# Kernel tuning notes

Measured on AMD Instinct MI355X. Metric: run time of the kernel, lower is better.

## Reference

```python
import jax, jax.numpy as jnp
import numpy as np

A_BITS = 7   # activation - 1, per T_quantize(norm(x), activation-1)
W_BITS = 7   # weight quantization levels bits (IRlinear, bit=weight)
HEADS = 16
DIM_HEAD = 64
LN_EPS = 1e-5


def qfn(x, bit):
    """Symmetric per-tensor uniform quantization with straight-through estimator.
    bit >= 31 means bypass (fp path, matching weight/activation == 32 defaults)."""
    if bit >= 31:
        return x
    n = jnp.asarray(2.0 ** bit - 1.0, x.dtype)
    s = jnp.max(jnp.abs(x))
    s = jnp.where(s == 0, jnp.asarray(1.0, x.dtype), s)
    y = jnp.round(x / s * n) / n * s
    # STE: forward uses quantized value, gradient passes through unchanged
    return x + jax.lax.stop_gradient(y - x)


def setup_inputs() -> dict:
    key = jax.random.key(0)
    kx, kq, ko = jax.random.split(key, 3)
    B, N, C = 8, 1024, 1024
    inner = HEADS * DIM_HEAD  # 1024
    x = jax.random.normal(kx, (B, N, C), dtype=jnp.float32)
    gamma = jnp.ones((C,), dtype=jnp.float32)
    beta = jnp.zeros((C,), dtype=jnp.float32)
    W_qkv = jax.random.normal(kq, (3 * inner, C), dtype=jnp.float32) * 0.02
    W_out = jax.random.normal(ko, (C, inner), dtype=jnp.float32) * 0.02
    b_out = jnp.zeros((C,), dtype=jnp.float32)
    return {"x": x, "gamma": gamma, "beta": beta,
            "W_qkv": W_qkv, "W_out": W_out, "b_out": b_out}


def reference(x, gamma, beta, W_qkv, W_out, b_out):
    B, N, C = x.shape
    H, Dh = HEADS, DIM_HEAD
    # LayerNorm
    mu = jnp.mean(x, axis=-1, keepdims=True)
    var = jnp.mean(jnp.square(x - mu), axis=-1, keepdims=True)
    xn = (x - mu) * jax.lax.rsqrt(var + LN_EPS) * gamma + beta
    # activation quantization (T_quantize with activation-1 bits)
    xq = qfn(xn, A_BITS)
    # quantized QKV projection (IRlinear, no bias)
    qkv = jnp.einsum('bnc,oc->bno', xq, qfn(W_qkv, W_BITS))
    qkv = qkv.reshape(B, N, 3, H, Dh).transpose(2, 0, 3, 1, 4)  # [3,B,H,N,Dh]
    q, k, v = qkv[0], qkv[1], qkv[2]
    # scaled dot-product attention (dropout_p = 0)
    scale = Dh ** -0.5
    scores = jnp.einsum('bhqd,bhkd->bhqk', q, k) * scale
    attn = jax.nn.softmax(scores, axis=-1)
    o = jnp.einsum('bhqk,bhkd->bhqd', attn, v)  # [B,H,N,Dh]
    o = o.transpose(0, 2, 1, 3).reshape(B, N, H * Dh)
    # quantized output projection (IRlinear, with bias)
    out = jnp.einsum('bni,ci->bnc', o, qfn(W_out, W_BITS)) + b_out
    return out
```

## Files before the change

kernel.cpp:

```cpp
#include <hip/hip_runtime.h>
#include <hip/hip_bf16.h>
#include <math.h>

typedef unsigned int u32;
typedef unsigned short u16;
using f32x4  = __attribute__((ext_vector_type(4))) float;
using f32x16 = __attribute__((ext_vector_type(16))) float;
using bfrag  = __attribute__((ext_vector_type(8))) short;
using i32x4  = __attribute__((ext_vector_type(4))) int;
union FragU { uint4 u; bfrag f; };
union FragI { uint4 u; i32x4 f; };

#define HEADS 16
#define DH    64
#define NB    8
#define NN    1024
#define NC    1024
#define M_TOT 8192
#define O_QKV 3072
#define KDIM  1024
#define LOG2E 1.44269504088896340736f

static __device__ __forceinline__ u16 f2bf(float f) {
  u32 u = __float_as_uint(f);
  return (u16)((u + 0x7fffu + ((u >> 16) & 1u)) >> 16);
}
static __device__ __forceinline__ u32 pk_bf16(float a, float b) {
  __hip_bfloat162 h = __float22bfloat162_rn(make_float2(a, b));
  u32 r; __builtin_memcpy(&r, &h, 4); return r;
}

static __device__ __forceinline__ float wave_sum(float v) {
#pragma unroll
  for (int off = 32; off > 0; off >>= 1) v += __shfl_xor(v, off, 64);
  return v;
}
static __device__ __forceinline__ float wave_max(float v) {
#pragma unroll
  for (int off = 32; off > 0; off >>= 1) v = fmaxf(v, __shfl_xor(v, off, 64));
  return v;
}

static __device__ __forceinline__ f32x4 mfma16(FragU a, FragU b, f32x4 c) {
  return __builtin_amdgcn_mfma_f32_16x16x32_bf16(a.f, b.f, c, 0, 0, 0);
}
static __device__ __forceinline__ f32x16 mfma32(FragU a, FragU b, f32x16 c) {
  return __builtin_amdgcn_mfma_f32_32x32x16_bf16(a.f, b.f, c, 0, 0, 0);
}
static __device__ __forceinline__ i32x4 mfma16i(FragI a, FragI b, i32x4 c) {
  return __builtin_amdgcn_mfma_i32_16x16x64_i8(a.f, b.f, c, 0, 0, 0);
}

static __device__ __forceinline__ void pl32swap(u32& a, u32& b) {
#if __has_builtin(__builtin_amdgcn_permlane32_swap)
  using u32x2 = __attribute__((ext_vector_type(2))) unsigned int;
  u32x2 r = __builtin_amdgcn_permlane32_swap(a, b, false, false);
  a = r[0]; b = r[1];
#else
  asm volatile("v_permlane32_swap_b32 %0, %1" : "+v"(a), "+v"(b));
#endif
}

template<int P, int BLK>
static __device__ __forceinline__ void stage_rows(const char* g, int row_stride,
                                                  char* ldsb, int t) {
#pragma unroll
  for (int p = 0; p < P; ++p) {
    const int c = p * BLK + t;
    const int row = c >> 3, kc = c & 7;
    const char* gp = g + (size_t)row * row_stride + ((kc ^ (row & 7)) << 4);
    char* lp = ldsb + ((p * BLK + (t & ~63)) << 4);
    __builtin_amdgcn_global_load_lds((const __attribute__((address_space(1))) void*)gp,
                                     (__attribute__((address_space(3))) void*)lp, 16, 0, 0);
  }
}
static __device__ __forceinline__ uint4 ld_chunk(const char* base, int row, int chunk) {
  return *(const uint4*)(base + (((row << 3) + (chunk ^ (row & 7))) << 4));
}

__global__ __launch_bounds__(256) void prep_kernel(const float* __restrict__ x,
    const float* __restrict__ g, const float* __restrict__ b,
    const float4* __restrict__ wq, const float4* __restrict__ wo,
    float2* __restrict__ mrs, float* __restrict__ actp,
    float* __restrict__ wqp, float* __restrict__ wop)
{
  __shared__ float red[4];
  const int bid = blockIdx.x, t = threadIdx.x;
  if (bid < 2048) {
    const int w = t >> 6, l = t & 63;
    const int row = (bid << 2) + w;
    const float4* xr = (const float4*)(x + (size_t)row * NC);
    float4 v[4];
#pragma unroll
    for (int j = 0; j < 4; ++j) v[j] = xr[l + (j << 6)];
    float s = 0.f;
#pragma unroll
    for (int j = 0; j < 4; ++j) s += (v[j].x + v[j].y) + (v[j].z + v[j].w);
    s = wave_sum(s);
    const float mu = s * (1.0f / NC);
    float ss = 0.f;
#pragma unroll
    for (int j = 0; j < 4; ++j) {
      const float dx = v[j].x - mu, dy = v[j].y - mu, dz = v[j].z - mu, dw = v[j].w - mu;
      ss += (dx * dx + dy * dy) + (dz * dz + dw * dw);
    }
    ss = wave_sum(ss);
    const float rstd = 1.0f / sqrtf(ss * (1.0f / NC) + 1e-5f);
    if (l == 0) mrs[row] = make_float2(mu, rstd);
    float am = 0.f;
#pragma unroll
    for (int j = 0; j < 4; ++j) {
      const float4 gv = ((const float4*)g)[l + (j << 6)];
      const float4 bv = ((const float4*)b)[l + (j << 6)];
      const float yx = (v[j].x - mu) * rstd * gv.x + bv.x;
      const float yy = (v[j].y - mu) * rstd * gv.y + bv.y;
      const float yz = (v[j].z - mu) * rstd * gv.z + bv.z;
      const float yw = (v[j].w - mu) * rstd * gv.w + bv.w;
      am = fmaxf(am, fmaxf(fmaxf(fabsf(yx), fabsf(yy)), fmaxf(fabsf(yz), fabsf(yw))));
    }
    am = wave_max(am);
    if (l == 0) red[w] = am;
    __syncthreads();
    if (t == 0) actp[bid] = fmaxf(fmaxf(red[0], red[1]), fmaxf(red[2], red[3]));
  } else {
    const float4* p; int n4, lb, nb; float* o;
    if (bid < 2560) { p = wq; n4 = O_QKV * KDIM / 4; lb = bid - 2048; nb = 512; o = wqp + lb; }
    else            { p = wo; n4 = NC * KDIM / 4;    lb = bid - 2560; nb = 256; o = wop + lb; }
    float m = 0.f;
    for (int i = lb * 256 + t; i < n4; i += nb * 256) {
      float4 v = p[i];
      m = fmaxf(m, fmaxf(fmaxf(fabsf(v.x), fabsf(v.y)), fmaxf(fabsf(v.z), fabsf(v.w))));
    }
    m = wave_max(m);
    if ((t & 63) == 0) red[t >> 6] = m;
    __syncthreads();
    if (t == 0) *o = fmaxf(fmaxf(red[0], red[1]), fmaxf(red[2], red[3]));
  }
}

__global__ __launch_bounds__(256) void reduce3(const float* __restrict__ actp,
    const float* __restrict__ wqp, const float* __restrict__ wop,
    unsigned* __restrict__ scal)
{
  const int t = threadIdx.x;
  float a = 0.f, q = 0.f, o = 0.f;
#pragma unroll
  for (int k = 0; k < 8; ++k) a = fmaxf(a, actp[t + (k << 8)]);
  q = fmaxf(wqp[t], wqp[t + 256]);
  o = wop[t];
  a = wave_max(a); q = wave_max(q); o = wave_max(o);
  __shared__ float ra[4], rq[4], ro[4];
  if ((t & 63) == 0) { ra[t >> 6] = a; rq[t >> 6] = q; ro[t >> 6] = o; }
  __syncthreads();
  if (t == 0) {
    a = fmaxf(fmaxf(ra[0], ra[1]), fmaxf(ra[2], ra[3]));
    q = fmaxf(fmaxf(rq[0], rq[1]), fmaxf(rq[2], rq[3]));
    o = fmaxf(fmaxf(ro[0], ro[1]), fmaxf(ro[2], ro[3]));
    scal[0] = __float_as_uint(a == 0.f ? 1.f : a);
    scal[1] = __float_as_uint(q == 0.f ? 1.f : q);
    scal[2] = __float_as_uint(o == 0.f ? 1.f : o);
  }
}

__global__ __launch_bounds__(256) void quant_all(const float* __restrict__ x,
    const float* __restrict__ g, const float* __restrict__ b,
    const float2* __restrict__ mrs, const unsigned* __restrict__ scal,
    u32* __restrict__ xq, const float4* __restrict__ wq, u32* __restrict__ oq,
    const float4* __restrict__ wo, uint2* __restrict__ oo)
{
  const int bid = blockIdx.x, t = threadIdx.x;
  if (bid < 8192) {
    const long long row = bid;
    const float2 ms = mrs[row];
    const float s = __uint_as_float(scal[0]);
    const float4 v = ((const float4*)(x + row * NC))[t];
    const float4 gv = ((const float4*)g)[t];
    const float4 bv = ((const float4*)b)[t];
    float4 y;
    y.x = (v.x - ms.x) * ms.y * gv.x + bv.x;
    y.y = (v.y - ms.x) * ms.y * gv.y + bv.y;
    y.z = (v.z - ms.x) * ms.y * gv.z + bv.z;
    y.w = (v.w - ms.x) * ms.y * gv.w + bv.w;
    const int ia = (int)rintf(y.x / s * 127.0f);
    const int ib = (int)rintf(y.y / s * 127.0f);
    const int ic = (int)rintf(y.z / s * 127.0f);
    const int id = (int)rintf(y.w / s * 127.0f);
    xq[row * 256 + t] = (u32)(ia & 255) | ((u32)(ib & 255) << 8)
                      | ((u32)(ic & 255) << 16) | ((u32)(id & 255) << 24);
  } else if (bid < 8960) {
    const float s = __uint_as_float(scal[1]);
    const int base = (bid - 8192) << 10;
#pragma unroll
    for (int k = 0; k < 4; ++k) {
      const int i = base + (k << 8) + t;
      float4 v = wq[i];
      const int ia = (int)rintf(v.x / s * 127.0f);
      const int ib = (int)rintf(v.y / s * 127.0f);
      const int ic = (int)rintf(v.z / s * 127.0f);
      const int id = (int)rintf(v.w / s * 127.0f);
      oq[i] = (u32)(ia & 255) | ((u32)(ib & 255) << 8)
            | ((u32)(ic & 255) << 16) | ((u32)(id & 255) << 24);
    }
  } else {
    const float s = __uint_as_float(scal[2]);
    const int base = (bid - 8960) << 10;
#pragma unroll
    for (int k = 0; k < 4; ++k) {
      const int i = base + (k << 8) + t;
      float4 v = wo[i];
      uint2 o;
      o.x = pk_bf16(rintf(v.x / s * 127.0f), rintf(v.y / s * 127.0f));
      o.y = pk_bf16(rintf(v.z / s * 127.0f), rintf(v.w / s * 127.0f));
      oo[i] = o;
    }
  }
}

__global__ __launch_bounds__(256) void gemm_qkv_mfma(const char* __restrict__ A,
    const char* __restrict__ B, const unsigned* __restrict__ scal,
    u16* __restrict__ qp, u16* __restrict__ kp, u16* __restrict__ vtp)
{
  __shared__ __align__(16) char lds[32768];
  char* As = lds;
  char* Bs = lds + 16384;
  const int t = threadIdx.x, w = t >> 6, l = t & 63;
  const int lg = l >> 4, lc = l & 15;
  const int wm = (w >> 1) << 6, wn = (w & 1) << 6;
  i32x4 acc[4][4];
#pragma unroll
  for (int i = 0; i < 4; ++i)
#pragma unroll
    for (int j = 0; j < 4; ++j) acc[i][j] = 0;

  const char* gA = A + ((size_t)blockIdx.y << 7) * KDIM;
  const char* gB = B + ((size_t)blockIdx.x << 7) * KDIM;

  for (int k0 = 0; k0 < KDIM; k0 += 128) {
    stage_rows<4, 256>(gA + k0, KDIM, As, t);
    stage_rows<4, 256>(gB + k0, KDIM, Bs, t);
    __syncthreads();
#pragma unroll
    for (int ks = 0; ks < 2; ++ks) {
      FragI a[4], b[4];
#pragma unroll
      for (int mf = 0; mf < 4; ++mf) a[mf].u = ld_chunk(As, wm + (mf << 4) + lc, (ks << 2) + lg);
#pragma unroll
      for (int nf = 0; nf < 4; ++nf) b[nf].u = ld_chunk(Bs, wn + (nf << 4) + lc, (ks << 2) + lg);
      __builtin_amdgcn_s_setprio(1);
#pragma unroll
      for (int mf = 0; mf < 4; ++mf)
#pragma unroll
        for (int nf = 0; nf < 4; ++nf) acc[mf][nf] = mfma16i(a[mf], b[nf], acc[mf][nf]);
      __builtin_amdgcn_s_setprio(0);
    }
    __syncthreads();
  }

  const float sa = __uint_as_float(scal[0]), sw = __uint_as_float(scal[1]);
  const int which = blockIdx.x >> 3;
  float sc = sa * sw / 16129.0f;
  if (which == 0) sc *= 0.125f * LOG2E;
  const int obase = ((blockIdx.x & 7) << 7) + wn;
  const int mbase = ((int)blockIdx.y << 7) + wm;

  if (which < 2) {
    u16* d_ = which ? kp : qp;
#pragma unroll
    for (int nf = 0; nf < 4; ++nf) {
      const int od = obase + (nf << 4) + lc;
      const int hh = od >> 6, dd = od & 63;
#pragma unroll
      for (int mf = 0; mf < 4; ++mf)
#pragma unroll
        for (int r = 0; r < 4; ++r) {
          const int tok = mbase + (mf << 4) + (lg << 2) + r;
          const size_t addr = ((size_t)((tok >> 10) * HEADS + hh) << 16)
                            + ((size_t)(tok & 1023) << 6) + dd;
          d_[addr] = f2bf((float)acc[mf][nf][r] * sc);
        }
    }
  } else {
#pragma unroll
    for (int nf = 0; nf < 4; ++nf) {
      const int od = obase + (nf << 4) + lc;
      const int hh = od >> 6, dd = od & 63;
#pragma unroll
      for (int mf = 0; mf < 4; ++mf) {
        const int tok0 = mbase + (mf << 4) + (lg << 2);
        uint2 hv;
        hv.x = pk_bf16((float)acc[mf][nf][0] * sc, (float)acc[mf][nf][1] * sc);
        hv.y = pk_bf16((float)acc[mf][nf][2] * sc, (float)acc[mf][nf][3] * sc);
        const size_t base = ((size_t)((tok0 >> 10) * HEADS + hh) << 16)
                          + ((size_t)dd << 10) + (tok0 & 1023);
        *(uint2*)(vtp + base) = hv;
      }
    }
  }
}

__global__ __launch_bounds__(512) void attn_mfma(
    const u16* __restrict__ qp, const u16* __restrict__ kp, const u16* __restrict__ vtp,
    u16* __restrict__ ohp)
{
  __shared__ __align__(16) char lds[65536];
  const int t = threadIdx.x, w = t >> 6, l = t & 63;
  const int l31 = l & 31, h = l >> 5;
  const int id = blockIdx.x;
  const int bh = ((id & 7) << 4) + ((id >> 3) & 15);
  const int qbase = ((id >> 7) << 8) + (w << 5);
  const size_t bhoff = (size_t)bh << 16;

  FragU qf[4];
#pragma unroll
  for (int ks = 0; ks < 4; ++ks)
    qf[ks].u = *(const uint4*)(qp + bhoff + ((size_t)(qbase + l31) << 6) + (ks << 4) + (h << 3));

  f32x16 oacc[2];
  oacc[0] = 0.f; oacc[1] = 0.f;
  float lpart = 0.f;

  stage_rows<2, 512>((const char*)(kp + bhoff), 128, lds, t);
  stage_rows<1, 512>((const char*)(vtp + bhoff), 2048, lds + 16384, t);
  stage_rows<1, 512>((const char*)(vtp + bhoff + 64), 2048, lds + 24576, t);
  __syncthreads();

  for (int kb = 0; kb < 8; ++kb) {
    char* cur = lds + ((kb & 1) << 15);
    if (kb < 7) {
      char* nxt = lds + (((kb + 1) & 1) << 15);
      const size_t kn = kb + 1;
      stage_rows<2, 512>((const char*)(kp + bhoff + (kn << 13)), 128, nxt, t);
      stage_rows<1, 512>((const char*)(vtp + bhoff + (kn << 7)), 2048, nxt + 16384, t);
      stage_rows<1, 512>((const char*)(vtp + bhoff + (kn << 7) + 64), 2048, nxt + 24576, t);
    }

#pragma unroll
    for (int sub = 0; sub < 4; ++sub) {
      f32x16 s = 0.f;
#pragma unroll
      for (int ks = 0; ks < 4; ++ks) {
        FragU kf;
        kf.u = ld_chunk(cur, (sub << 5) + l31, (ks << 1) + h);
        __builtin_amdgcn_s_setprio(1);
        s = mfma32(kf, qf[ks], s);
        __builtin_amdgcn_s_setprio(0);
      }

      u32 W[8];
      float lsum = 0.f;
#pragma unroll
      for (int j = 0; j < 8; ++j) {
        const float a = __builtin_amdgcn_exp2f(s[2 * j]);
        const float b = __builtin_amdgcn_exp2f(s[2 * j + 1]);
        lsum += a + b;
        W[j] = pk_bf16(a, b);
      }
      lpart += lsum;

      FragU pf[2];
#pragma unroll
      for (int kk = 0; kk < 2; ++kk) {
        u32 a0 = W[4 * kk + 0], b0 = W[4 * kk + 2];
        u32 a1 = W[4 * kk + 1], b1 = W[4 * kk + 3];
        pl32swap(a0, b0); pl32swap(a1, b1);
        pf[kk].u = make_uint4(a0, a1, b0, b1);
      }

      char* Vh = cur + 16384 + ((sub >> 1) << 13);
#pragma unroll
      for (int ks = 0; ks < 2; ++ks)
#pragma unroll
        for (int dt = 0; dt < 2; ++dt) {
          FragU vf;
          vf.u = ld_chunk(Vh, (dt << 5) + l31, ((sub & 1) << 2) + (ks << 1) + h);
          __builtin_amdgcn_s_setprio(1);
          oacc[dt] = mfma32(vf, pf[ks], oacc[dt]);
          __builtin_amdgcn_s_setprio(0);
        }
    }
    __syncthreads();
  }

  lpart += __shfl_xor(lpart, 32, 64);
  const float invl = 1.0f / lpart;

  const int b = bh >> 4, hd_ = bh & 15;
  const size_t orow = (size_t)b * NN + qbase + l31;
  u16* ohb = ohp + (orow << 10) + (hd_ << 6);
#pragma unroll
  for (int dt = 0; dt < 2; ++dt)
#pragma unroll
    for (int rg = 0; rg < 4; ++rg) {
      const int d0 = (dt << 5) + (rg << 3) + (h << 2);
      const float v0 = oacc[dt][4 * rg + 0] * invl, v1 = oacc[dt][4 * rg + 1] * invl;
      const float v2 = oacc[dt][4 * rg + 2] * invl, v3 = oacc[dt][4 * rg + 3] * invl;
      uint2 hv;
      hv.x = (u32)f2bf(v0) | ((u32)f2bf(v1) << 16);
      hv.y = (u32)f2bf(v2) | ((u32)f2bf(v3) << 16);
      *(uint2*)(ohb + d0) = hv;
    }
}

__global__ __launch_bounds__(256) void gemm_out_mfma(const u16* __restrict__ Ah,
    const u16* __restrict__ B, const unsigned* __restrict__ scal,
    const float* __restrict__ bias, float* __restrict__ out)
{
  __shared__ __align__(16) char lds[32768];
  char* Ahs = lds;
  char* Bs  = lds + 16384;
  const int t = threadIdx.x, w = t >> 6, l = t & 63;
  const int lg = l >> 4, lc = l & 15;
  const int wm = (w >> 1) << 6, wn = (w & 1) << 6;
  f32x4 acc[4][4];
#pragma unroll
  for (int i = 0; i < 4; ++i)
#pragma unroll
    for (int j = 0; j < 4; ++j) acc[i][j] = 0.f;

  const char* gAh = (const char*)Ah + ((size_t)blockIdx.y << 7) * 2048;
  const char* gB  = (const char*)B  + ((size_t)blockIdx.x << 7) * 2048;

  for (int k0 = 0; k0 < KDIM; k0 += 64) {
    stage_rows<4, 256>(gAh + k0 * 2, 2048, Ahs, t);
    stage_rows<4, 256>(gB  + k0 * 2, 2048, Bs,  t);
    __syncthreads();
#pragma unroll
    for (int ks = 0; ks < 2; ++ks) {
      FragU a[4], b[4];
#pragma unroll
      for (int mf = 0; mf < 4; ++mf) a[mf].u = ld_chunk(Ahs, wm + (mf << 4) + lc, (ks << 2) + lg);
#pragma unroll
      for (int nf = 0; nf < 4; ++nf) b[nf].u = ld_chunk(Bs, wn + (nf << 4) + lc, (ks << 2) + lg);
      __builtin_amdgcn_s_setprio(1);
#pragma unroll
      for (int mf = 0; mf < 4; ++mf)
#pragma unroll
        for (int nf = 0; nf < 4; ++nf) acc[mf][nf] = mfma16(a[mf], b[nf], acc[mf][nf]);
      __builtin_amdgcn_s_setprio(0);
    }
    __syncthreads();
  }

  const float sc = __uint_as_float(scal[2]) / 127.0f;
  const int cb = ((int)blockIdx.x << 7) + wn;
  const int mb = ((int)blockIdx.y << 7) + wm;
#pragma unroll
  for (int nf = 0; nf < 4; ++nf) {
    const int col = cb + (nf << 4) + lc;
    const float bv = bias[col];
#pragma unroll
    for (int mf = 0; mf < 4; ++mf)
#pragma unroll
      for (int r = 0; r < 4; ++r) {
        const int row = mb + (mf << 4) + (lg << 2) + r;
        out[(size_t)row * NC + col] = acc[mf][nf][r] * sc + bv;
      }
  }
}

__global__ void ws_fail_kernel(float* out) { out[0] = 1.0e6f; }

extern "C" void kernel_launch(void* const* d_in, const int* in_sizes, int n_in,
                              void* d_out, int out_size, void* d_ws, size_t ws_size,
                              hipStream_t stream) {
  const float* x     = (const float*)d_in[0];
  const float* gamma = (const float*)d_in[1];
  const float* beta  = (const float*)d_in[2];
  const float* Wqkv  = (const float*)d_in[3];
  const float* Wout  = (const float*)d_in[4];
  const float* bout  = (const float*)d_in[5];
  float* out = (float*)d_out;

  char* ws = (char*)d_ws;
  unsigned* scal = (unsigned*)ws;
  size_t off = 256;
  float* actp = (float*)(ws + off); off += 2048 * 4;
  float* wqp  = (float*)(ws + off); off += 512 * 4;
  float* wop  = (float*)(ws + off); off += 256 * 4;
  off = (off + 255) & ~(size_t)255;
  float2* mrs = (float2*)(ws + off); off += (size_t)M_TOT * 8;
  char* xq  = ws + off; off += (size_t)M_TOT * KDIM;
  char* wqi = ws + off; off += (size_t)O_QKV * KDIM;
  u16* woi = (u16*)(ws + off); off += (size_t)NC * KDIM * 2;
  u16* qb  = (u16*)(ws + off); off += 16777216;
  u16* kb  = (u16*)(ws + off); off += 16777216;
  u16* vtb = (u16*)(ws + off); off += 16777216;
  u16* oh  = (u16*)(ws + off); off += 16777216;
  if (ws_size < off) { ws_fail_kernel<<<1, 1, 0, stream>>>(out); return; }

  prep_kernel<<<2816, 256, 0, stream>>>(x, gamma, beta, (const float4*)Wqkv,
                                        (const float4*)Wout, mrs, actp, wqp, wop);
  reduce3<<<1, 256, 0, stream>>>(actp, wqp, wop, scal);
  quant_all<<<9216, 256, 0, stream>>>(x, gamma, beta, mrs, scal, (u32*)xq,
                                      (const float4*)Wqkv, (u32*)wqi,
                                      (const float4*)Wout, (uint2*)woi);

  dim3 g1(O_QKV / 128, M_TOT / 128);
  gemm_qkv_mfma<<<g1, 256, 0, stream>>>(xq, wqi, scal, qb, kb, vtb);

  attn_mfma<<<512, 512, 0, stream>>>(qb, kb, vtb, oh);

  dim3 g3(NC / 128, M_TOT / 128);
  gemm_out_mfma<<<g3, 256, 0, stream>>>(oh, woi, scal, bout, out);
}
```

Baseline: 139.2 us.

## Fold scale reduction into quant kernel, transpose Q/K MFMA for packed stores, stagger attention subtiles

Removes the separate single-block reduce3 launch: each quant_all block now redundantly reduces the partial maxima itself, and block 0 writes the scalars for the later GEMMs. The QKV GEMM swaps MFMA operand order for the Q/K outputs so each lane holds four consecutive head-dim values and can write packed 8-byte stores instead of scalar 2-byte stores. The attention kernel rotates the sub-tile order per wave, likely to spread LDS bank accesses. Each quant block now does extra redundant reduction reads, and a duplicated GEMM loop adds code size.

```diff
diff --git a/kernel.cpp b/kernel.cpp
--- a/kernel.cpp
+++ b/kernel.cpp
@@ -76,6 +76,19 @@
 }
 static __device__ __forceinline__ uint4 ld_chunk(const char* base, int row, int chunk) {
   return *(const uint4*)(base + (((row << 3) + (chunk ^ (row & 7))) << 4));
+}
+
+static __device__ __forceinline__ float blk_max4(const float4* p, int n4, int t, float* red) {
+  float m = 0.f;
+  for (int i = t; i < n4; i += 256) {
+    float4 v = p[i];
+    m = fmaxf(m, fmaxf(fmaxf(v.x, v.y), fmaxf(v.z, v.w)));
+  }
+  m = wave_max(m);
+  __syncthreads();
+  if ((t & 63) == 0) red[t >> 6] = m;
+  __syncthreads();
+  return fmaxf(fmaxf(red[0], red[1]), fmaxf(red[2], red[3]));
 }
 
 __global__ __launch_bounds__(256) void prep_kernel(const float* __restrict__ x,
@@ -138,41 +151,30 @@
   }
 }
 
-__global__ __launch_bounds__(256) void reduce3(const float* __restrict__ actp,
-    const float* __restrict__ wqp, const float* __restrict__ wop,
-    unsigned* __restrict__ scal)
-{
-  const int t = threadIdx.x;
-  float a = 0.f, q = 0.f, o = 0.f;
-#pragma unroll
-  for (int k = 0; k < 8; ++k) a = fmaxf(a, actp[t + (k << 8)]);
-  q = fmaxf(wqp[t], wqp[t + 256]);
-  o = wop[t];
-  a = wave_max(a); q = wave_max(q); o = wave_max(o);
-  __shared__ float ra[4], rq[4], ro[4];
-  if ((t & 63) == 0) { ra[t >> 6] = a; rq[t >> 6] = q; ro[t >> 6] = o; }
-  __syncthreads();
-  if (t == 0) {
-    a = fmaxf(fmaxf(ra[0], ra[1]), fmaxf(ra[2], ra[3]));
-    q = fmaxf(fmaxf(rq[0], rq[1]), fmaxf(rq[2], rq[3]));
-    o = fmaxf(fmaxf(ro[0], ro[1]), fmaxf(ro[2], ro[3]));
-    scal[0] = __float_as_uint(a == 0.f ? 1.f : a);
-    scal[1] = __float_as_uint(q == 0.f ? 1.f : q);
-    scal[2] = __float_as_uint(o == 0.f ? 1.f : o);
-  }
-}
-
 __global__ __launch_bounds__(256) void quant_all(const float* __restrict__ x,
     const float* __restrict__ g, const float* __restrict__ b,
-    const float2* __restrict__ mrs, const unsigned* __restrict__ scal,
+    const float2* __restrict__ mrs,
+    const float* __restrict__ actp, const float* __restrict__ wqp,
+    const float* __restrict__ wop, unsigned* __restrict__ scal,
     u32* __restrict__ xq, const float4* __restrict__ wq, u32* __restrict__ oq,
     const float4* __restrict__ wo, uint2* __restrict__ oo)
 {
+  __shared__ float red[4];
   const int bid = blockIdx.x, t = threadIdx.x;
   if (bid < 8192) {
+    float s = blk_max4((const float4*)actp, 512, t, red);
+    if (s == 0.f) s = 1.f;
+    if (bid == 0) {
+      float qm = blk_max4((const float4*)wqp, 128, t, red);
+      float om = blk_max4((const float4*)wop, 64, t, red);
+      if (t == 0) {
+        scal[0] = __float_as_uint(s);
+        scal[1] = __float_as_uint(qm == 0.f ? 1.f : qm);
+        scal[2] = __float_as_uint(om == 0.f ? 1.f : om);
+      }
+    }
     const long long row = bid;
     const float2 ms = mrs[row];
-    const float s = __uint_as_float(scal[0]);
     const float4 v = ((const float4*)(x + row * NC))[t];
     const float4 gv = ((const float4*)g)[t];
     const float4 bv = ((const float4*)b)[t];
@@ -188,7 +190,8 @@
     xq[row * 256 + t] = (u32)(ia & 255) | ((u32)(ib & 255) << 8)
                       | ((u32)(ic & 255) << 16) | ((u32)(id & 255) << 24);
   } else if (bid < 8960) {
-    const float s = __uint_as_float(scal[1]);
+    float s = blk_max4((const float4*)wqp, 128, t, red);
+    if (s == 0.f) s = 1.f;
     const int base = (bid - 8192) << 10;
 #pragma unroll
     for (int k = 0; k < 4; ++k) {
@@ -202,7 +205,8 @@
             | ((u32)(ic & 255) << 16) | ((u32)(id & 255) << 24);
     }
   } else {
-    const float s = __uint_as_float(scal[2]);
+    float s = blk_max4((const float4*)wop, 64, t, red);
+    if (s == 0.f) s = 1.f;
     const int base = (bid - 8960) << 10;
 #pragma unroll
     for (int k = 0; k < 4; ++k) {
@@ -226,6 +230,7 @@
   const int t = threadIdx.x, w = t >> 6, l = t & 63;
   const int lg = l >> 4, lc = l & 15;
   const int wm = (w >> 1) << 6, wn = (w & 1) << 6;
+  const int which = blockIdx.x >> 3;
   i32x4 acc[4][4];
 #pragma unroll
   for (int i = 0; i < 4; ++i)
@@ -235,29 +240,51 @@
   const char* gA = A + ((size_t)blockIdx.y << 7) * KDIM;
   const char* gB = B + ((size_t)blockIdx.x << 7) * KDIM;
 
-  for (int k0 = 0; k0 < KDIM; k0 += 128) {
-    stage_rows<4, 256>(gA + k0, KDIM, As, t);
-    stage_rows<4, 256>(gB + k0, KDIM, Bs, t);
-    __syncthreads();
-#pragma unroll
-    for (int ks = 0; ks < 2; ++ks) {
-      FragI a[4], b[4];
-#pragma unroll
-      for (int mf = 0; mf < 4; ++mf) a[mf].u = ld_chunk(As, wm + (mf << 4) + lc, (ks << 2) + lg);
-#pragma unroll
-      for (int nf = 0; nf < 4; ++nf) b[nf].u = ld_chunk(Bs, wn + (nf << 4) + lc, (ks << 2) + lg);
-      __builtin_amdgcn_s_setprio(1);
-#pragma unroll
-      for (int mf = 0; mf < 4; ++mf)
-#pragma unroll
-        for (int nf = 0; nf < 4; ++nf) acc[mf][nf] = mfma16i(a[mf], b[nf], acc[mf][nf]);
-      __builtin_amdgcn_s_setprio(0);
-    }
-    __syncthreads();
+  if (which < 2) {
+    for (int k0 = 0; k0 < KDIM; k0 += 128) {
+      stage_rows<4, 256>(gA + k0, KDIM, As, t);
+      stage_rows<4, 256>(gB + k0, KDIM, Bs, t);
+      __syncthreads();
+#pragma unroll
+      for (int ks = 0; ks < 2; ++ks) {
+        FragI a[4], b[4];
+#pragma unroll
+        for (int mf = 0; mf < 4; ++mf) a[mf].u = ld_chunk(As, wm + (mf << 4) + lc, (ks << 2) + lg);
+#pragma unroll
+        for (int nf = 0; nf < 4; ++nf) b[nf].u = ld_chunk(Bs, wn + (nf << 4) + lc, (ks << 2) + lg);
+        __builtin_amdgcn_s_setprio(1);
+#pragma unroll
+        for (int wf = 0; wf < 4; ++wf)
+#pragma unroll
+          for (int tf = 0; tf < 4; ++tf) acc[wf][tf] = mfma16i(b[wf], a[tf], acc[wf][tf]);
+        __builtin_amdgcn_s_setprio(0);
+      }
+      __syncthreads();
+    }
+  } else {
+    for (int k0 = 0; k0 < KDIM; k0 += 128) {
+      stage_rows<4, 256>(gA + k0, KDIM, As, t);
+      stage_rows<4, 256>(gB + k0, KDIM, Bs, t);
+      __syncthreads();
+#pragma unroll
+      for (int ks = 0; ks < 2; ++ks) {
+        FragI a[4], b[4];
+#pragma unroll
+        for (int mf = 0; mf < 4; ++mf) a[mf].u = ld_chunk(As, wm + (mf << 4) + lc, (ks << 2) + lg);
+#pragma unroll
+        for (int nf = 0; nf < 4; ++nf) b[nf].u = ld_chunk(Bs, wn + (nf << 4) + lc, (ks << 2) + lg);
+        __builtin_amdgcn_s_setprio(1);
+#pragma unroll
+        for (int mf = 0; mf < 4; ++mf)
+#pragma unroll
+          for (int nf = 0; nf < 4; ++nf) acc[mf][nf] = mfma16i(a[mf], b[nf], acc[mf][nf]);
+        __builtin_amdgcn_s_setprio(0);
+      }
+      __syncthreads();
+    }
   }
 
   const float sa = __uint_as_float(scal[0]), sw = __uint_as_float(scal[1]);
-  const int which = blockIdx.x >> 3;
   float sc = sa * sw / 16129.0f;
   if (which == 0) sc *= 0.125f * LOG2E;
   const int obase = ((blockIdx.x & 7) << 7) + wn;
@@ -266,18 +293,19 @@
   if (which < 2) {
     u16* d_ = which ? kp : qp;
 #pragma unroll
-    for (int nf = 0; nf < 4; ++nf) {
-      const int od = obase + (nf << 4) + lc;
-      const int hh = od >> 6, dd = od & 63;
-#pragma unroll
-      for (int mf = 0; mf < 4; ++mf)
-#pragma unroll
-        for (int r = 0; r < 4; ++r) {
-          const int tok = mbase + (mf << 4) + (lg << 2) + r;
-          const size_t addr = ((size_t)((tok >> 10) * HEADS + hh) << 16)
-                            + ((size_t)(tok & 1023) << 6) + dd;
-          d_[addr] = f2bf((float)acc[mf][nf][r] * sc);
-        }
+    for (int wf = 0; wf < 4; ++wf) {
+      const int od0 = obase + (wf << 4) + (lg << 2);
+      const int hh = od0 >> 6, dd = od0 & 63;
+#pragma unroll
+      for (int tf = 0; tf < 4; ++tf) {
+        const int tok = mbase + (tf << 4) + lc;
+        uint2 hv;
+        hv.x = pk_bf16((float)acc[wf][tf][0] * sc, (float)acc[wf][tf][1] * sc);
+        hv.y = pk_bf16((float)acc[wf][tf][2] * sc, (float)acc[wf][tf][3] * sc);
+        const size_t addr = ((size_t)((tok >> 10) * HEADS + hh) << 16)
+                          + ((size_t)(tok & 1023) << 6) + dd;
+        *(uint2*)(d_ + addr) = hv;
+      }
     }
   } else {
 #pragma unroll
@@ -335,7 +363,8 @@
     }
 
 #pragma unroll
-    for (int sub = 0; sub < 4; ++sub) {
+    for (int sp = 0; sp < 4; ++sp) {
+      const int sub = (sp + w) & 3;
       f32x16 s = 0.f;
 #pragma unroll
       for (int ks = 0; ks < 4; ++ks) {
@@ -490,9 +519,8 @@
 
   prep_kernel<<<2816, 256, 0, stream>>>(x, gamma, beta, (const float4*)Wqkv,
                                         (const float4*)Wout, mrs, actp, wqp, wop);
-  reduce3<<<1, 256, 0, stream>>>(actp, wqp, wop, scal);
-  quant_all<<<9216, 256, 0, stream>>>(x, gamma, beta, mrs, scal, (u32*)xq,
-                                      (const float4*)Wqkv, (u32*)wqi,
+  quant_all<<<9216, 256, 0, stream>>>(x, gamma, beta, mrs, actp, wqp, wop, scal,
+                                      (u32*)xq, (const float4*)Wqkv, (u32*)wqi,
                                       (const float4*)Wout, (uint2*)woi);
 
   dim3 g1(O_QKV / 128, M_TOT / 128);
```

Result: slower. 158.3 us (+13.8%).
